# Kernel optimization log

Hardware: AMD Instinct MI355X
Metric: run time of the kernel (lower is better)

Reference implementation:

```python
import jax, jax.numpy as jnp
import numpy as np

NUM_TRUE = 8
NUM_NULL = 2
NUM_EXPERTS = NUM_TRUE + NUM_NULL
TOP_K = 2


def setup_inputs() -> dict:
    key = jax.random.key(0)
    k0, k1, k2 = jax.random.split(key, 3)
    B, S, D = 4, 2048, 1024
    inputs = jax.random.normal(k0, (B, S, D), dtype=jnp.float32)
    gate_w = jax.random.normal(k1, (NUM_EXPERTS, D), dtype=jnp.float32) * 0.02
    gate_b = jnp.zeros((NUM_EXPERTS,), dtype=jnp.float32)
    # expert_w stored as [E, D_in, D_out] so expert i computes x @ expert_w[i] + expert_b[i]
    expert_w = jax.random.normal(k2, (NUM_TRUE, D, D), dtype=jnp.float32) * 0.02
    expert_b = jnp.zeros((NUM_TRUE, D), dtype=jnp.float32)
    return {"inputs": inputs, "gate_w": gate_w, "gate_b": gate_b,
            "expert_w": expert_w, "expert_b": expert_b}


def reference(inputs, gate_w, gate_b, expert_w, expert_b):
    D = inputs.shape[-1]
    x = inputs.reshape(-1, D)                       # [T, D]
    gate_logits = x @ gate_w.T + gate_b             # [T, E]
    gate_probs = jax.nn.softmax(gate_logits, axis=-1)
    weights, selected = jax.lax.top_k(gate_probs, TOP_K)  # [T, K]
    true_mask = selected < NUM_TRUE                 # null experts contribute nothing
    true_weights = weights * true_mask
    denom = true_weights.sum(axis=-1, keepdims=True)
    denom = jnp.where(denom > 0, denom, jnp.ones_like(denom))
    norm_w = (true_weights / denom).astype(x.dtype)  # [T, K]
    # per-(token, true-expert) combine weight; zero for unselected experts
    one_hot = jax.nn.one_hot(selected, NUM_EXPERTS, dtype=norm_w.dtype)  # [T, K, E]
    combine_w = jnp.einsum('tk,tke->te', norm_w, one_hot)[:, :NUM_TRUE]  # [T, E_true]
    # dense expert evaluation, then weighted combine (zero weights cancel
    # exactly as the gather/scatter loop in the torch code)
    expert_out = jnp.einsum('td,edh->teh', x, expert_w) + expert_b[None, :, :]  # [T, E_true, D]
    out = jnp.einsum('te,teh->th', combine_w, expert_out)  # [T, D]
    return out.reshape(inputs.shape[:-1] + (out.shape[-1],))
```

## Files before the change

kernel.cpp:

```cpp
#include <hip/hip_runtime.h>
#include <hip/hip_bf16.h>
#include <stdint.h>

#define T_TOKENS 8192
#define D_DIM    1024
#define NE       10
#define NT       8
#define SEG      2048

typedef unsigned short u16;
typedef __attribute__((ext_vector_type(8))) __bf16 bf16x8;
typedef __attribute__((ext_vector_type(4))) float  f32x4;
typedef __attribute__((ext_vector_type(8))) unsigned short u16x8;
typedef __attribute__((ext_vector_type(4))) unsigned short u16x4;

static __device__ __forceinline__ u16 f32_to_bf16(float f) {
  union { float f; uint32_t u; } v; v.f = f;
  uint32_t u = v.u;
  return (u16)((u + 0x7fffu + ((u >> 16) & 1u)) >> 16);
}
static __device__ __forceinline__ float bf16_to_f32(u16 u) {
  union { uint32_t u; float f; } v; v.u = ((uint32_t)u) << 16; return v.f;
}

static __device__ __forceinline__ void async_load16(const u16* g, u16* l) {
  __builtin_amdgcn_global_load_lds(
      (const __attribute__((address_space(1))) void*)(const void*)g,
      (__attribute__((address_space(3))) void*)(void*)l, 16, 0, 0);
}

__global__ __launch_bounds__(256) void gate_kernel(
    const float* __restrict__ x, const float* __restrict__ gw,
    const float* __restrict__ gb, u16* __restrict__ xb,
    int* __restrict__ cnt, int* __restrict__ tokList,
    int* __restrict__ revIdx, float* __restrict__ revW) {
  __shared__ float gws[NE * D_DIM];
  __shared__ float gbs[NE];
  __shared__ int   se[32];
  __shared__ float swt[32];
  int tid = threadIdx.x;
  {
    const f32x4* g4 = (const f32x4*)gw;
    f32x4* s4 = (f32x4*)gws;
    for (int i = tid; i < NE * D_DIM / 4; i += 256) s4[i] = g4[i];
  }
  if (tid < NE) gbs[tid] = gb[tid];
  __syncthreads();
  int lane = tid & 63;
  int wv   = tid >> 6;
  const f32x4* gws4 = (const f32x4*)gws;
  for (int it = 0; it < 4; ++it) {
    int slot = wv * 4 + it;
    int t = blockIdx.x * 16 + slot;
    const f32x4* xr4 = (const f32x4*)(x + (size_t)t * D_DIM);
    f32x4 xv[4];
#pragma unroll
    for (int jj = 0; jj < 4; ++jj) xv[jj] = xr4[lane + 64 * jj];
    u16x4* xbr = (u16x4*)(xb + (size_t)t * D_DIM);
#pragma unroll
    for (int jj = 0; jj < 4; ++jj) {
      u16x4 pk;
#pragma unroll
      for (int k = 0; k < 4; ++k) pk[k] = f32_to_bf16(xv[jj][k]);
      xbr[lane + 64 * jj] = pk;
    }
    float logit[NE];
#pragma unroll
    for (int e = 0; e < NE; ++e) {
      float a = 0.f;
#pragma unroll
      for (int jj = 0; jj < 4; ++jj) {
        f32x4 gv = gws4[e * 256 + lane + 64 * jj];
#pragma unroll
        for (int k = 0; k < 4; ++k) a = fmaf(xv[jj][k], gv[k], a);
      }
#pragma unroll
      for (int off = 32; off >= 1; off >>= 1) a += __shfl_xor(a, off);
      logit[e] = a + gbs[e];
    }
    float mx = logit[0];
#pragma unroll
    for (int e = 1; e < NE; ++e) mx = fmaxf(mx, logit[e]);
    float p[NE]; float s = 0.f;
#pragma unroll
    for (int e = 0; e < NE; ++e) { p[e] = expf(logit[e] - mx); s += p[e]; }
    int e0 = 0; float b0 = p[0];
#pragma unroll
    for (int e = 1; e < NE; ++e) if (p[e] > b0) { b0 = p[e]; e0 = e; }
    int e1 = -1; float b1 = -1.f;
#pragma unroll
    for (int e = 0; e < NE; ++e) if (e != e0 && p[e] > b1) { b1 = p[e]; e1 = e; }
    float w0 = b0 / s, w1 = b1 / s;
    float tw0 = (e0 < NT) ? w0 : 0.f;
    float tw1 = (e1 < NT) ? w1 : 0.f;
    float denom = tw0 + tw1;
    float nw0 = 0.f, nw1 = 0.f;
    if (denom > 0.f) { nw0 = tw0 / denom; nw1 = tw1 / denom; }
    if (lane == 0) {
      se[slot * 2]     = (e0 < NT) ? e0 : -1;  swt[slot * 2]     = nw0;
      se[slot * 2 + 1] = (e1 < NT) ? e1 : -1;  swt[slot * 2 + 1] = nw1;
      if (e0 >= NT) { revIdx[t * 2]     = -1; revW[t * 2]     = 0.f; }
      if (e1 >= NT) { revIdx[t * 2 + 1] = -1; revW[t * 2 + 1] = 0.f; }
    }
  }
  __syncthreads();
  if (tid < NT) {
    int e = tid, c = 0;
    for (int i = 0; i < 32; ++i) c += (se[i] == e);
    if (c > 0) {
      int base = atomicAdd(&cnt[e * 32], c);
      int j = 0;
      for (int i = 0; i < 32; ++i) {
        if (se[i] == e) {
          int tt  = blockIdx.x * 16 + (i >> 1);
          int pos = base + j;
          tokList[e * SEG + pos]   = tt;
          revIdx[tt * 2 + (i & 1)] = e * SEG + pos;
          revW[tt * 2 + (i & 1)]   = swt[i];
          ++j;
        }
      }
    }
  }
}

__global__ __launch_bounds__(256) void transpose_w(
    const float* __restrict__ W, u16* __restrict__ wT) {
  __shared__ float tile[64][65];
  int e  = blockIdx.z;
  int k0 = blockIdx.y * 64;
  int n0 = blockIdx.x * 64;
  int c  = threadIdx.x & 63;
  int r0 = threadIdx.x >> 6;
  const float* We = W + ((size_t)e << 20);
#pragma unroll
  for (int rr = 0; rr < 16; ++rr) {
    int r = rr * 4 + r0;
    tile[c][r] = We[(size_t)(k0 + r) * 1024 + n0 + c];
  }
  __syncthreads();
  u16* wTe = wT + ((size_t)e << 20);
#pragma unroll
  for (int rr = 0; rr < 16; ++rr) {
    int n = rr * 4 + r0;
    wTe[(size_t)(n0 + n) * 1024 + k0 + c] = f32_to_bf16(tile[n][c]);
  }
}

__global__ __launch_bounds__(256) void moe_gemm(
    const u16* __restrict__ xb, const u16* __restrict__ wT,
    const int* __restrict__ cnt, const int* __restrict__ tokList,
    const float* __restrict__ eb, u16* __restrict__ ybuf) {
  int e  = blockIdx.x;
  int c  = cnt[e * 32];
  int m0 = blockIdx.z * 128;
  if (m0 >= c) return;
  int n0 = blockIdx.y * 128;
  __shared__ __align__(16) u16 As[2][128 * 32];
  __shared__ __align__(16) u16 Bs[2][128 * 32];
  __shared__ int tokS[128];
  int tid = threadIdx.x;
  if (tid < 128) {
    int gm = m0 + tid;
    tokS[tid] = (gm < c) ? tokList[e * SEG + gm] : tokList[e * SEG];
  }
  __syncthreads();
  int lane = tid & 63;
  int wv   = tid >> 6;
  int rl  = lane >> 2;
  int kcp = lane & 3;
  int kcd = kcp ^ (rl & 3);
  int rowL0 = wv * 32 + rl, rowL1 = rowL0 + 16;
  const u16* gA0 = xb + (size_t)tokS[rowL0] * 1024 + kcd * 8;
  const u16* gA1 = xb + (size_t)tokS[rowL1] * 1024 + kcd * 8;
  const u16* wTe = wT + ((size_t)e << 20);
  const u16* gB0 = wTe + (size_t)(n0 + rowL0) * 1024 + kcd * 8;
  const u16* gB1 = wTe + (size_t)(n0 + rowL1) * 1024 + kcd * 8;

  int wm = wv >> 1, wn = wv & 1;
  int lrow = lane & 15;
  int q    = lane >> 4;
  int sw   = (q ^ (lrow & 3)) * 8;
  f32x4 acc[4][4];
#pragma unroll
  for (int i = 0; i < 4; ++i)
#pragma unroll
    for (int j = 0; j < 4; ++j) acc[i][j] = (f32x4){0.f, 0.f, 0.f, 0.f};

  async_load16(gA0, As[0] + (wv * 32) * 32);
  async_load16(gA1, As[0] + (wv * 32 + 16) * 32);
  async_load16(gB0, Bs[0] + (wv * 32) * 32);
  async_load16(gB1, Bs[0] + (wv * 32 + 16) * 32);

  for (int kt = 0; kt < 32; ++kt) {
    int cur = kt & 1;
    if (kt < 31) {
      asm volatile("s_barrier" ::: "memory");
      int ko = (kt + 1) * 32;
      async_load16(gA0 + ko, As[1 - cur] + (wv * 32) * 32);
      async_load16(gA1 + ko, As[1 - cur] + (wv * 32 + 16) * 32);
      async_load16(gB0 + ko, Bs[1 - cur] + (wv * 32) * 32);
      async_load16(gB1 + ko, Bs[1 - cur] + (wv * 32 + 16) * 32);
      asm volatile("s_waitcnt vmcnt(4)" ::: "memory");
    } else {
      asm volatile("s_waitcnt vmcnt(0)" ::: "memory");
    }
    asm volatile("s_barrier" ::: "memory");
    bf16x8 af[4], bfr[4];
#pragma unroll
    for (int mt = 0; mt < 4; ++mt)
      af[mt] = *(const bf16x8*)(As[cur] + (wm * 64 + mt * 16 + lrow) * 32 + sw);
#pragma unroll
    for (int nt = 0; nt < 4; ++nt)
      bfr[nt] = *(const bf16x8*)(Bs[cur] + (wn * 64 + nt * 16 + lrow) * 32 + sw);
#pragma unroll
    for (int mt = 0; mt < 4; ++mt)
#pragma unroll
      for (int nt = 0; nt < 4; ++nt)
        acc[mt][nt] = __builtin_amdgcn_mfma_f32_16x16x32_bf16(
            af[mt], bfr[nt], acc[mt][nt], 0, 0, 0);
  }
  int rq = lane >> 4;
  float bias[4];
#pragma unroll
  for (int nt = 0; nt < 4; ++nt)
    bias[nt] = eb[e * 1024 + n0 + wn * 64 + nt * 16 + lrow];
  u16* yb = ybuf + ((size_t)(e * SEG + m0)) * 1024 + n0 + wn * 64 + lrow;
#pragma unroll
  for (int mt = 0; mt < 4; ++mt) {
#pragma unroll
    for (int r = 0; r < 4; ++r) {
      int ml = wm * 64 + mt * 16 + rq * 4 + r;
      u16* row = yb + (size_t)ml * 1024;
#pragma unroll
      for (int nt = 0; nt < 4; ++nt)
        row[nt * 16] = f32_to_bf16(acc[mt][nt][r] + bias[nt]);
    }
  }
}

__global__ __launch_bounds__(256) void combine_kernel(
    const u16* __restrict__ ybuf, const int* __restrict__ revIdx,
    const float* __restrict__ revW, float* __restrict__ out) {
  int tid = threadIdx.x, lane = tid & 63, wv = tid >> 6;
  for (int it = 0; it < 4; ++it) {
    int t  = blockIdx.x * 16 + wv * 4 + it;
    int i0 = revIdx[t * 2], i1 = revIdx[t * 2 + 1];
    float w0 = revW[t * 2], w1 = revW[t * 2 + 1];
    float o[16];
#pragma unroll
    for (int k = 0; k < 16; ++k) o[k] = 0.f;
    if (i0 >= 0) {
      const u16x8* y = (const u16x8*)(ybuf + (size_t)i0 * 1024);
#pragma unroll
      for (int jj = 0; jj < 2; ++jj) {
        u16x8 v = y[lane + 64 * jj];
#pragma unroll
        for (int k = 0; k < 8; ++k) o[jj * 8 + k] += w0 * bf16_to_f32(v[k]);
      }
    }
    if (i1 >= 0) {
      const u16x8* y = (const u16x8*)(ybuf + (size_t)i1 * 1024);
#pragma unroll
      for (int jj = 0; jj < 2; ++jj) {
        u16x8 v = y[lane + 64 * jj];
#pragma unroll
        for (int k = 0; k < 8; ++k) o[jj * 8 + k] += w1 * bf16_to_f32(v[k]);
      }
    }
    f32x4* o4 = (f32x4*)(out + (size_t)t * 1024);
#pragma unroll
    for (int jj = 0; jj < 2; ++jj)
#pragma unroll
      for (int h = 0; h < 2; ++h) {
        f32x4 vv = {o[jj * 8 + h * 4], o[jj * 8 + h * 4 + 1],
                    o[jj * 8 + h * 4 + 2], o[jj * 8 + h * 4 + 3]};
        o4[2 * (lane + 64 * jj) + h] = vv;
      }
  }
}

extern "C" void kernel_launch(void* const* d_in, const int* in_sizes, int n_in,
                              void* d_out, int out_size, void* d_ws, size_t ws_size,
                              hipStream_t stream) {
  const float* x  = (const float*)d_in[0];
  const float* gw = (const float*)d_in[1];
  const float* gb = (const float*)d_in[2];
  const float* ew = (const float*)d_in[3];
  const float* eb = (const float*)d_in[4];
  float* out = (float*)d_out;
  char* ws = (char*)d_ws;
  int*   cnt     = (int*)ws;
  int*   tokList = (int*)(ws + 4096);
  int*   revIdx  = (int*)(ws + 4096 + 65536);
  float* revW    = (float*)(ws + 4096 + 131072);
  u16*   xb      = (u16*)(ws + 200704);
  u16*   wT      = (u16*)(ws + 200704 + 16777216);
  u16*   ybuf    = (u16*)(ws + 200704 + 33554432);

  hipMemsetAsync(cnt, 0, 4096, stream);
  gate_kernel<<<512, 256, 0, stream>>>(x, gw, gb, xb, cnt, tokList, revIdx, revW);
  transpose_w<<<dim3(16, 16, 8), 256, 0, stream>>>(ew, wT);
  moe_gemm<<<dim3(8, 8, 16), 256, 0, stream>>>(xb, wT, cnt, tokList, eb, ybuf);
  combine_kernel<<<512, 256, 0, stream>>>(ybuf, revIdx, revW, out);
}
```

Before: 188.0 us.

## Merge gate and weight transpose into one launch; triple-buffer GEMM loads

The gate and weight-transpose kernels are merged into a single prep kernel whose block index selects the role, with a shared-memory union. This removes one launch and lets both independent jobs run on the GPU at once. The expert GEMM moves from double to triple buffering of LDS tiles, prefetching two k-steps ahead with adjusted vmcnt waits to hide more global-load latency. The cost is more LDS per GEMM block, which may lower occupancy, and the prep kernel's shared allocation is now sized for the larger gate layout even in transpose blocks.

```diff
diff --git a/kernel.cpp b/kernel.cpp
--- a/kernel.cpp
+++ b/kernel.cpp
@@ -29,26 +29,54 @@
       (__attribute__((address_space(3))) void*)(void*)l, 16, 0, 0);
 }
 
-__global__ __launch_bounds__(256) void gate_kernel(
+union PrepShared {
+  struct { float gws[NE * D_DIM]; float gbs[NE]; int se[32]; float swt[32]; } g;
+  struct { float tile[64][65]; } t;
+};
+
+__global__ __launch_bounds__(256) void prep_kernel(
     const float* __restrict__ x, const float* __restrict__ gw,
-    const float* __restrict__ gb, u16* __restrict__ xb,
+    const float* __restrict__ gb, const float* __restrict__ W,
+    u16* __restrict__ xb, u16* __restrict__ wT,
     int* __restrict__ cnt, int* __restrict__ tokList,
     int* __restrict__ revIdx, float* __restrict__ revW) {
-  __shared__ float gws[NE * D_DIM];
-  __shared__ float gbs[NE];
-  __shared__ int   se[32];
-  __shared__ float swt[32];
+  __shared__ PrepShared sh;
   int tid = threadIdx.x;
+
+  if (blockIdx.x >= 512) {
+    int tb = blockIdx.x - 512;
+    int e  = tb >> 8;
+    int rem = tb & 255;
+    int k0 = (rem >> 4) * 64;
+    int n0 = (rem & 15) * 64;
+    int c  = tid & 63;
+    int r0 = tid >> 6;
+    const float* We = W + ((size_t)e << 20);
+#pragma unroll
+    for (int rr = 0; rr < 16; ++rr) {
+      int r = rr * 4 + r0;
+      sh.t.tile[c][r] = We[(size_t)(k0 + r) * 1024 + n0 + c];
+    }
+    __syncthreads();
+    u16* wTe = wT + ((size_t)e << 20);
+#pragma unroll
+    for (int rr = 0; rr < 16; ++rr) {
+      int n = rr * 4 + r0;
+      wTe[(size_t)(n0 + n) * 1024 + k0 + c] = f32_to_bf16(sh.t.tile[n][c]);
+    }
+    return;
+  }
+
   {
     const f32x4* g4 = (const f32x4*)gw;
-    f32x4* s4 = (f32x4*)gws;
+    f32x4* s4 = (f32x4*)sh.g.gws;
     for (int i = tid; i < NE * D_DIM / 4; i += 256) s4[i] = g4[i];
   }
-  if (tid < NE) gbs[tid] = gb[tid];
+  if (tid < NE) sh.g.gbs[tid] = gb[tid];
   __syncthreads();
   int lane = tid & 63;
   int wv   = tid >> 6;
-  const f32x4* gws4 = (const f32x4*)gws;
+  const f32x4* gws4 = (const f32x4*)sh.g.gws;
   for (int it = 0; it < 4; ++it) {
     int slot = wv * 4 + it;
     int t = blockIdx.x * 16 + slot;
@@ -76,7 +104,7 @@
       }
 #pragma unroll
       for (int off = 32; off >= 1; off >>= 1) a += __shfl_xor(a, off);
-      logit[e] = a + gbs[e];
+      logit[e] = a + sh.g.gbs[e];
     }
     float mx = logit[0];
 #pragma unroll
@@ -97,8 +125,8 @@
     float nw0 = 0.f, nw1 = 0.f;
     if (denom > 0.f) { nw0 = tw0 / denom; nw1 = tw1 / denom; }
     if (lane == 0) {
-      se[slot * 2]     = (e0 < NT) ? e0 : -1;  swt[slot * 2]     = nw0;
-      se[slot * 2 + 1] = (e1 < NT) ? e1 : -1;  swt[slot * 2 + 1] = nw1;
+      sh.g.se[slot * 2]     = (e0 < NT) ? e0 : -1;  sh.g.swt[slot * 2]     = nw0;
+      sh.g.se[slot * 2 + 1] = (e1 < NT) ? e1 : -1;  sh.g.swt[slot * 2 + 1] = nw1;
       if (e0 >= NT) { revIdx[t * 2]     = -1; revW[t * 2]     = 0.f; }
       if (e1 >= NT) { revIdx[t * 2 + 1] = -1; revW[t * 2 + 1] = 0.f; }
     }
@@ -106,44 +134,21 @@
   __syncthreads();
   if (tid < NT) {
     int e = tid, c = 0;
-    for (int i = 0; i < 32; ++i) c += (se[i] == e);
+    for (int i = 0; i < 32; ++i) c += (sh.g.se[i] == e);
     if (c > 0) {
       int base = atomicAdd(&cnt[e * 32], c);
       int j = 0;
       for (int i = 0; i < 32; ++i) {
-        if (se[i] == e) {
+        if (sh.g.se[i] == e) {
           int tt  = blockIdx.x * 16 + (i >> 1);
           int pos = base + j;
           tokList[e * SEG + pos]   = tt;
           revIdx[tt * 2 + (i & 1)] = e * SEG + pos;
-          revW[tt * 2 + (i & 1)]   = swt[i];
+          revW[tt * 2 + (i & 1)]   = sh.g.swt[i];
           ++j;
         }
       }
     }
-  }
-}
-
-__global__ __launch_bounds__(256) void transpose_w(
-    const float* __restrict__ W, u16* __restrict__ wT) {
-  __shared__ float tile[64][65];
-  int e  = blockIdx.z;
-  int k0 = blockIdx.y * 64;
-  int n0 = blockIdx.x * 64;
-  int c  = threadIdx.x & 63;
-  int r0 = threadIdx.x >> 6;
-  const float* We = W + ((size_t)e << 20);
-#pragma unroll
-  for (int rr = 0; rr < 16; ++rr) {
-    int r = rr * 4 + r0;
-    tile[c][r] = We[(size_t)(k0 + r) * 1024 + n0 + c];
-  }
-  __syncthreads();
-  u16* wTe = wT + ((size_t)e << 20);
-#pragma unroll
-  for (int rr = 0; rr < 16; ++rr) {
-    int n = rr * 4 + r0;
-    wTe[(size_t)(n0 + n) * 1024 + k0 + c] = f32_to_bf16(tile[n][c]);
   }
 }
 
@@ -156,8 +161,8 @@
   int m0 = blockIdx.z * 128;
   if (m0 >= c) return;
   int n0 = blockIdx.y * 128;
-  __shared__ __align__(16) u16 As[2][128 * 32];
-  __shared__ __align__(16) u16 Bs[2][128 * 32];
+  __shared__ __align__(16) u16 As[3][128 * 32];
+  __shared__ __align__(16) u16 Bs[3][128 * 32];
   __shared__ int tokS[128];
   int tid = threadIdx.x;
   if (tid < 128) {
@@ -176,6 +181,7 @@
   const u16* wTe = wT + ((size_t)e << 20);
   const u16* gB0 = wTe + (size_t)(n0 + rowL0) * 1024 + kcd * 8;
   const u16* gB1 = wTe + (size_t)(n0 + rowL1) * 1024 + kcd * 8;
+  int ldsA0 = (wv * 32) * 32, ldsA1 = (wv * 32 + 16) * 32;
 
   int wm = wv >> 1, wn = wv & 1;
   int lrow = lane & 15;
@@ -187,20 +193,27 @@
 #pragma unroll
     for (int j = 0; j < 4; ++j) acc[i][j] = (f32x4){0.f, 0.f, 0.f, 0.f};
 
-  async_load16(gA0, As[0] + (wv * 32) * 32);
-  async_load16(gA1, As[0] + (wv * 32 + 16) * 32);
-  async_load16(gB0, Bs[0] + (wv * 32) * 32);
-  async_load16(gB1, Bs[0] + (wv * 32 + 16) * 32);
-
+#pragma unroll
+  for (int p = 0; p < 2; ++p) {
+    int ko = p * 32;
+    async_load16(gA0 + ko, As[p] + ldsA0);
+    async_load16(gA1 + ko, As[p] + ldsA1);
+    async_load16(gB0 + ko, Bs[p] + ldsA0);
+    async_load16(gB1 + ko, Bs[p] + ldsA1);
+  }
+
+  int cur = 0;
   for (int kt = 0; kt < 32; ++kt) {
-    int cur = kt & 1;
-    if (kt < 31) {
-      asm volatile("s_barrier" ::: "memory");
-      int ko = (kt + 1) * 32;
-      async_load16(gA0 + ko, As[1 - cur] + (wv * 32) * 32);
-      async_load16(gA1 + ko, As[1 - cur] + (wv * 32 + 16) * 32);
-      async_load16(gB0 + ko, Bs[1 - cur] + (wv * 32) * 32);
-      async_load16(gB1 + ko, Bs[1 - cur] + (wv * 32 + 16) * 32);
+    asm volatile("s_barrier" ::: "memory");
+    if (kt < 30) {
+      int st = cur - 1; if (st < 0) st += 3;
+      int ko = (kt + 2) * 32;
+      async_load16(gA0 + ko, As[st] + ldsA0);
+      async_load16(gA1 + ko, As[st] + ldsA1);
+      async_load16(gB0 + ko, Bs[st] + ldsA0);
+      async_load16(gB1 + ko, Bs[st] + ldsA1);
+      asm volatile("s_waitcnt vmcnt(8)" ::: "memory");
+    } else if (kt == 30) {
       asm volatile("s_waitcnt vmcnt(4)" ::: "memory");
     } else {
       asm volatile("s_waitcnt vmcnt(0)" ::: "memory");
@@ -219,6 +232,7 @@
       for (int nt = 0; nt < 4; ++nt)
         acc[mt][nt] = __builtin_amdgcn_mfma_f32_16x16x32_bf16(
             af[mt], bfr[nt], acc[mt][nt], 0, 0, 0);
+    ++cur; if (cur == 3) cur = 0;
   }
   int rq = lane >> 4;
   float bias[4];
@@ -299,8 +313,8 @@
   u16*   ybuf    = (u16*)(ws + 200704 + 33554432);
 
   hipMemsetAsync(cnt, 0, 4096, stream);
-  gate_kernel<<<512, 256, 0, stream>>>(x, gw, gb, xb, cnt, tokList, revIdx, revW);
-  transpose_w<<<dim3(16, 16, 8), 256, 0, stream>>>(ew, wT);
+  prep_kernel<<<2560, 256, 0, stream>>>(x, gw, gb, ew, xb, wT, cnt, tokList,
+                                        revIdx, revW);
   moe_gemm<<<dim3(8, 8, 16), 256, 0, stream>>>(xb, wT, cnt, tokList, eb, ybuf);
   combine_kernel<<<512, 256, 0, stream>>>(ybuf, revIdx, revW, out);
 }
```

New measurement: 177.4 us. 1.06x faster.
